# Performance work log

Measured on AMD Instinct MI355X. Metric: run time of the kernel, lower is better.

The kernel has to match this reference:

```python
import jax, jax.numpy as jnp
import numpy as np

EPS = 1e-5
N_NODES = 100000


def setup_inputs() -> dict:
    key = jax.random.key(0)
    ks = jax.random.split(key, 24)
    N, F = N_NODES, 64
    E = 1600000
    inp = {
        "x": jax.random.normal(ks[0], (N, F), dtype=jnp.float32),
        "edge_index": jax.random.randint(ks[1], (2, E), 0, N, dtype=jnp.int64),
    }
    dims = [(F, 32), (32, 64), (64, 128), (128, 1)]
    for i, (din, dout) in enumerate(dims, start=1):
        kw, kb = jax.random.split(ks[1 + i], 2)
        scale = 1.0 / np.sqrt(din)
        inp[f"W{i}"] = jax.random.uniform(kw, (din, dout), jnp.float32, -scale, scale)
        inp[f"b{i}"] = jax.random.uniform(kb, (dout,), jnp.float32, -scale, scale)
    for i, d in enumerate([32, 64, 128], start=1):
        kg, kbe, km, kv = jax.random.split(ks[8 + i], 4)
        inp[f"g{i}"] = 1.0 + 0.1 * jax.random.normal(kg, (d,), jnp.float32)
        inp[f"be{i}"] = 0.1 * jax.random.normal(kbe, (d,), jnp.float32)
        inp[f"rm{i}"] = 0.1 * jax.random.normal(km, (d,), jnp.float32)
        inp[f"rv{i}"] = 0.5 + jax.random.uniform(kv, (d,), jnp.float32)
    return inp


def _gcn_conv(x, src, dst, norm, W, b, n):
    # GCNConv: linear transform then D^-1/2 A_hat D^-1/2 aggregation (self-loops in src/dst)
    xw = x @ W  # [N, dout]
    msg = xw[src] * norm[:, None]  # [E+N, dout] gather
    return jax.ops.segment_sum(msg, dst, num_segments=n) + b


def _bn_eval(x, g, be, rm, rv):
    return (x - rm) * jax.lax.rsqrt(rv + EPS) * g + be


def reference(x, edge_index, W1, b1, W2, b2, W3, b3, W4, b4,
              g1, be1, rm1, rv1, g2, be2, rm2, rv2, g3, be3, rm3, rv3):
    n = x.shape[0]
    loop = jnp.arange(n, dtype=edge_index.dtype)
    src = jnp.concatenate([edge_index[0], loop])
    dst = jnp.concatenate([edge_index[1], loop])
    deg = jax.ops.segment_sum(jnp.ones_like(dst, dtype=x.dtype), dst, num_segments=n)
    dinv = jnp.where(deg > 0, jax.lax.rsqrt(deg), 0.0)
    norm = dinv[src] * dinv[dst]  # shared across layers

    h = _gcn_conv(x, src, dst, norm, W1, b1, n)
    h = jax.nn.elu(_bn_eval(h, g1, be1, rm1, rv1))
    h = _gcn_conv(h, src, dst, norm, W2, b2, n)
    h = jax.nn.elu(_bn_eval(h, g2, be2, rm2, rv2))
    h = _gcn_conv(h, src, dst, norm, W3, b3, n)
    h = jax.nn.elu(_bn_eval(h, g3, be3, rm3, rv3))
    h = _gcn_conv(h, src, dst, norm, W4, b4, n)
    return jax.nn.sigmoid(jax.nn.elu(h))
```

## Files before the change

kernel.cpp:

```cpp
#include <hip/hip_runtime.h>
#include <hip/hip_fp16.h>

#define EPSF 1e-5f
#define BKT_SHIFT 9
#define BKT_NODES 512
#define TILE_E 4096

typedef _Float16 half2_t __attribute__((ext_vector_type(2)));

__device__ __forceinline__ float elu_f(float x) { return x > 0.f ? x : expm1f(x); }

__device__ __forceinline__ float fdot2f(half2_t a, half2_t b, float c) {
#if __has_builtin(__builtin_amdgcn_fdot2)
    return __builtin_amdgcn_fdot2(a, b, c, false);
#else
    return c + (float)a.x * (float)b.x + (float)a.y * (float)b.y;
#endif
}
__device__ __forceinline__ half2_t bch2(unsigned u) { return __builtin_bit_cast(half2_t, u); }

__device__ __forceinline__ float4 h4_to_f4(uint2 u) {
    __half2 a = *reinterpret_cast<const __half2*>(&u.x);
    __half2 b = *reinterpret_cast<const __half2*>(&u.y);
    float2 fa = __half22float2(a);
    float2 fb = __half22float2(b);
    return make_float4(fa.x, fa.y, fb.x, fb.y);
}
__device__ __forceinline__ uint2 f4_to_h4(float4 v) {
    __half2 a = __floats2half2_rn(v.x, v.y);
    __half2 b = __floats2half2_rn(v.z, v.w);
    uint2 u;
    u.x = *reinterpret_cast<unsigned*>(&a);
    u.y = *reinterpret_cast<unsigned*>(&b);
    return u;
}


__global__ __launch_bounds__(256) void k_zero(int* p, int n) {
    int i = blockIdx.x * 256 + threadIdx.x;
    if (i < n) p[i] = 0;
}

__global__ __launch_bounds__(256) void k_bhist(const int* __restrict__ dst, int* __restrict__ bkt_cnt, int E) {
    __shared__ int h[256];
    int t = threadIdx.x;
    h[t] = 0;
    __syncthreads();
    for (long e = (long)blockIdx.x * 256 + t; e < E; e += (long)gridDim.x * 256)
        atomicAdd(&h[dst[e] >> BKT_SHIFT], 1);
    __syncthreads();
    if (h[t]) atomicAdd(&bkt_cnt[t], h[t]);
}

__global__ __launch_bounds__(256) void k_bscan(const int* __restrict__ bkt_cnt, int* __restrict__ bbase,
                                               int* __restrict__ cursor) {
    __shared__ int sh[256];
    int t = threadIdx.x;
    int v = bkt_cnt[t];
    sh[t] = v;
    __syncthreads();
    for (int off = 1; off < 256; off <<= 1) {
        int add = (t >= off) ? sh[t - off] : 0;
        __syncthreads();
        sh[t] += add;
        __syncthreads();
    }
    int ex = sh[t] - v;
    bbase[t] = ex;
    cursor[t] = ex;
}

__global__ __launch_bounds__(256) void k_bpart(const int* __restrict__ src, const int* __restrict__ dst,
                                               int* __restrict__ cursor, int2* __restrict__ csr_tmp, int E) {
    __shared__ int hcnt[256];
    __shared__ int gbase[256];
    int t = threadIdx.x;
    long tile0 = (long)blockIdx.x * TILE_E;
    hcnt[t] = 0;
    __syncthreads();
    int d[16], s[16], rk[16];
    #pragma unroll
    for (int j = 0; j < 16; ++j) {
        long e = tile0 + j * 256 + t;
        if (e < E) {
            d[j] = dst[e];
            s[j] = src[e];
            rk[j] = atomicAdd(&hcnt[d[j] >> BKT_SHIFT], 1);
        }
    }
    __syncthreads();
    int c = hcnt[t];
    if (c) gbase[t] = atomicAdd(&cursor[t], c);
    __syncthreads();
    #pragma unroll
    for (int j = 0; j < 16; ++j) {
        long e = tile0 + j * 256 + t;
        if (e < E) {
            int2 q;
            q.x = d[j];
            q.y = s[j];
            csr_tmp[gbase[d[j] >> BKT_SHIFT] + rk[j]] = q;
        }
    }
}

__global__ __launch_bounds__(256) void k_bfine(const int2* __restrict__ csr_tmp, const int* __restrict__ bbase,
                                               const int* __restrict__ bkt_cnt, int* __restrict__ cnt,
                                               int* __restrict__ base, float* __restrict__ dinv,
                                               int* __restrict__ csr_s, int N) {
    __shared__ int cnt5[BKT_NODES];
    __shared__ int off5[BKT_NODES];
    __shared__ int sh[256];
    int b = blockIdx.x;
    int t = threadIdx.x;
    int d0 = b << BKT_SHIFT;
    int bb = bbase[b];
    int bc = bkt_cnt[b];
    cnt5[t] = 0;
    cnt5[t + 256] = 0;
    __syncthreads();
    for (int k = t; k < bc; k += 256) atomicAdd(&cnt5[csr_tmp[bb + k].x - d0], 1);
    __syncthreads();
    int v0 = cnt5[2 * t], v1 = cnt5[2 * t + 1];
    int p = v0 + v1;
    sh[t] = p;
    __syncthreads();
    for (int off = 1; off < 256; off <<= 1) {
        int add = (t >= off) ? sh[t - off] : 0;
        __syncthreads();
        sh[t] += add;
        __syncthreads();
    }
    int pre = sh[t] - p;
    off5[2 * t] = pre;
    off5[2 * t + 1] = pre + v0;
    #pragma unroll
    for (int j = 0; j < 2; ++j) {
        int idx = 2 * t + j;
        int i = d0 + idx;
        if (i < N) {
            int c = cnt5[idx];
            base[i] = bb + off5[idx];
            cnt[i] = c;
            dinv[i] = rsqrtf((float)(c + 1));
        }
    }
    __syncthreads();
    for (int k = t; k < bc; k += 256) {
        int2 e = csr_tmp[bb + k];
        int pos = bb + atomicAdd(&off5[e.x - d0], 1);
        csr_s[pos] = e.y;
    }
}

template<int F, bool L1EPI, bool HIN, bool HOUT>
__global__ __launch_bounds__(256) void k_gather(const int* __restrict__ base, const int* __restrict__ cnt,
                                                const int* __restrict__ csr_s,
                                                const float* __restrict__ dinv, const void* __restrict__ xin,
                                                const float* __restrict__ b, const float* __restrict__ g,
                                                const float* __restrict__ be, const float* __restrict__ rm,
                                                const float* __restrict__ rv, void* __restrict__ out, int n) {
    constexpr int C = F / 4;
    constexpr int NPB = 256 / C;
    int lane = threadIdx.x % C;
    int nl = threadIdx.x / C;
    int i = blockIdx.x * NPB + nl;
    if (i >= n) return;
    int k = base[i];
    int kend = k + cnt[i];
    float di = dinv[i];
    const float4* XF = reinterpret_cast<const float4*>(xin);
    const uint2*  XH = reinterpret_cast<const uint2*>(xin);
    float4 z = {0.f, 0.f, 0.f, 0.f};
    float4 a0 = z, a1 = z, a2 = z, a3 = z;
    for (; k + 3 < kend; k += 4) {
        int s0 = csr_s[k], s1 = csr_s[k + 1], s2 = csr_s[k + 2], s3 = csr_s[k + 3];
        float4 x0 = HIN ? h4_to_f4(XH[(long)s0 * C + lane]) : XF[(long)s0 * C + lane];
        float4 x1 = HIN ? h4_to_f4(XH[(long)s1 * C + lane]) : XF[(long)s1 * C + lane];
        float4 x2 = HIN ? h4_to_f4(XH[(long)s2 * C + lane]) : XF[(long)s2 * C + lane];
        float4 x3 = HIN ? h4_to_f4(XH[(long)s3 * C + lane]) : XF[(long)s3 * C + lane];
        a0.x += x0.x; a0.y += x0.y; a0.z += x0.z; a0.w += x0.w;
        a1.x += x1.x; a1.y += x1.y; a1.z += x1.z; a1.w += x1.w;
        a2.x += x2.x; a2.y += x2.y; a2.z += x2.z; a2.w += x2.w;
        a3.x += x3.x; a3.y += x3.y; a3.z += x3.z; a3.w += x3.w;
    }
    for (; k < kend; ++k) {
        int s0 = csr_s[k];
        float4 xa = HIN ? h4_to_f4(XH[(long)s0 * C + lane]) : XF[(long)s0 * C + lane];
        a0.x += xa.x; a0.y += xa.y; a0.z += xa.z; a0.w += xa.w;
    }
    float4 xs = HIN ? h4_to_f4(XH[(long)i * C + lane]) : XF[(long)i * C + lane];
    float4 o;
    o.x = di * (a0.x + a1.x + a2.x + a3.x + xs.x);
    o.y = di * (a0.y + a1.y + a2.y + a3.y + xs.y);
    o.z = di * (a0.z + a1.z + a2.z + a3.z + xs.z);
    o.w = di * (a0.w + a1.w + a2.w + a3.w + xs.w);
    if (L1EPI) {
        float4 bb = reinterpret_cast<const float4*>(b)[lane];
        float4 gg = reinterpret_cast<const float4*>(g)[lane];
        float4 ee = reinterpret_cast<const float4*>(be)[lane];
        float4 mm = reinterpret_cast<const float4*>(rm)[lane];
        float4 vv = reinterpret_cast<const float4*>(rv)[lane];
        o.x = di * elu_f((o.x + bb.x - mm.x) * rsqrtf(vv.x + EPSF) * gg.x + ee.x);
        o.y = di * elu_f((o.y + bb.y - mm.y) * rsqrtf(vv.y + EPSF) * gg.y + ee.y);
        o.z = di * elu_f((o.z + bb.z - mm.z) * rsqrtf(vv.z + EPSF) * gg.z + ee.z);
        o.w = di * elu_f((o.w + bb.w - mm.w) * rsqrtf(vv.w + EPSF) * gg.w + ee.w);
    }
    if (HOUT) reinterpret_cast<uint2*>(out)[(long)i * C + lane] = f4_to_h4(o);
    else      reinterpret_cast<float4*>(out)[(long)i * C + lane] = o;
}

__global__ __launch_bounds__(256) void k_gather1_final(const int* __restrict__ base, const int* __restrict__ cnt,
                                                       const int* __restrict__ csr_s,
                                                       const float* __restrict__ dinv, const float* __restrict__ y,
                                                       const float* __restrict__ b4, float* __restrict__ out, int n) {
    int i = blockIdx.x * 256 + threadIdx.x;
    if (i >= n) return;
    int k = base[i];
    int kend = k + cnt[i];
    float di = dinv[i];
    float acc = 0.f;
    for (; k < kend; ++k) acc += y[csr_s[k]];
    float v = di * (acc + y[i]) + b4[0];
    v = elu_f(v);
    out[i] = 1.f / (1.f + expf(-v));
}

template<int DIN, int DOUT, bool BN, bool FUSE_DOT, bool SCALE_DINV, bool HOUT>
__global__ __launch_bounds__(256, 4) void k_gemm_rt(const float* __restrict__ X, const float* __restrict__ W,
                                                    const float* __restrict__ b, const float* __restrict__ g,
                                                    const float* __restrict__ be, const float* __restrict__ rm,
                                                    const float* __restrict__ rv, const float* __restrict__ W4,
                                                    const float* __restrict__ dinv,
                                                    void* __restrict__ Y, int n) {
    constexpr int TR = 4;
    constexpr int FL = DOUT / 4;
    constexpr int RG = 256 / FL;
    constexpr int BR = RG * TR;
    __shared__ float Wl[DIN * DOUT];
    for (int idx = threadIdx.x; idx < DIN * DOUT; idx += 256) Wl[idx] = W[idx];
    __syncthreads();
    const int fl = threadIdx.x % FL;
    const int rg = threadIdx.x / FL;
    const int f0 = fl * 4;
    const long r0 = (long)blockIdx.x * BR + (long)rg * TR;

    float4 z; z.x = z.y = z.z = z.w = 0.f;
    float4 acc[TR];
    #pragma unroll
    for (int r = 0; r < TR; ++r) acc[r] = z;

    #pragma unroll 2
    for (int k0 = 0; k0 < DIN; k0 += 4) {
        float4 xv[TR];
        #pragma unroll
        for (int r = 0; r < TR; ++r) {
            long row = r0 + r;
            xv[r] = (row < n) ? *reinterpret_cast<const float4*>(X + row * DIN + k0) : z;
        }
        #pragma unroll
        for (int kk = 0; kk < 4; ++kk) {
            float4 w4 = *reinterpret_cast<const float4*>(&Wl[(k0 + kk) * DOUT + f0]);
            #pragma unroll
            for (int r = 0; r < TR; ++r) {
                float xs = (kk == 0) ? xv[r].x : (kk == 1) ? xv[r].y : (kk == 2) ? xv[r].z : xv[r].w;
                acc[r].x += xs * w4.x;
                acc[r].y += xs * w4.y;
                acc[r].z += xs * w4.z;
                acc[r].w += xs * w4.w;
            }
        }
    }

    float4 bias = z, scale = z, shift = z, w4d = z;
    if (BN) {
        bias = *reinterpret_cast<const float4*>(b + f0);
        float4 gg = *reinterpret_cast<const float4*>(g + f0);
        float4 ee = *reinterpret_cast<const float4*>(be + f0);
        float4 mm = *reinterpret_cast<const float4*>(rm + f0);
        float4 vv = *reinterpret_cast<const float4*>(rv + f0);
        scale.x = gg.x * rsqrtf(vv.x + EPSF); shift.x = ee.x - mm.x * scale.x;
        scale.y = gg.y * rsqrtf(vv.y + EPSF); shift.y = ee.y - mm.y * scale.y;
        scale.z = gg.z * rsqrtf(vv.z + EPSF); shift.z = ee.z - mm.z * scale.z;
        scale.w = gg.w * rsqrtf(vv.w + EPSF); shift.w = ee.w - mm.w * scale.w;
    }
    if (FUSE_DOT) w4d = *reinterpret_cast<const float4*>(W4 + f0);

    #pragma unroll
    for (int r = 0; r < TR; ++r) {
        long row = r0 + r;
        if (row >= n) continue;
        float4 v = acc[r];
        if (BN) {
            v.x = elu_f((v.x + bias.x) * scale.x + shift.x);
            v.y = elu_f((v.y + bias.y) * scale.y + shift.y);
            v.z = elu_f((v.z + bias.z) * scale.z + shift.z);
            v.w = elu_f((v.w + bias.w) * scale.w + shift.w);
        }
        float dv = SCALE_DINV ? dinv[row] : 1.f;
        if (FUSE_DOT) {
            float p = v.x * w4d.x + v.y * w4d.y + v.z * w4d.z + v.w * w4d.w;
            #pragma unroll
            for (int m = 1; m < FL; m <<= 1) p += __shfl_xor(p, m, 64);
            if (fl == 0) reinterpret_cast<float*>(Y)[row] = dv * p;
        } else {
            if (SCALE_DINV) { v.x *= dv; v.y *= dv; v.z *= dv; v.w *= dv; }
            if (HOUT) reinterpret_cast<uint2*>(Y)[row * FL + fl] = f4_to_h4(v);
            else      *reinterpret_cast<float4*>(reinterpret_cast<float*>(Y) + row * DOUT + f0) = v;
        }
    }
}

__global__ __launch_bounds__(256, 4) void k_fuse2(const int* __restrict__ base, const int* __restrict__ cnt,
                                                  const int* __restrict__ csr_s, const float* __restrict__ dinv,
                                                  const uint2* __restrict__ Xh,
                                                  const float* __restrict__ W, const float* __restrict__ b,
                                                  const float* __restrict__ g, const float* __restrict__ be,
                                                  const float* __restrict__ rm, const float* __restrict__ rv,
                                                  uint2* __restrict__ Y,
                                                  int n) {
    __shared__ half2_t Wl2[16 * 64];
    __shared__ __align__(16) uint2 T2[32 * 8];
    __shared__ float Dl[32];
    int t = threadIdx.x;
    for (int idx = t; idx < 16 * 64; idx += 256) {
        int p = idx >> 6, j = idx & 63;
        half2_t w;
        w.x = (_Float16)W[(2 * p) * 64 + j];
        w.y = (_Float16)W[(2 * p + 1) * 64 + j];
        Wl2[idx] = w;
    }
    int lane = t & 7, nl = t >> 3;
    long i = (long)blockIdx.x * 32 + nl;
    float4 z = {0.f, 0.f, 0.f, 0.f};
    float4 o = z;
    float di = 0.f;
    if (i < n) {
        int k = base[i], kend = k + cnt[i];
        di = dinv[i];
        float4 a0 = z, a1 = z;
        for (; k + 1 < kend; k += 2) {
            int s0 = csr_s[k], s1 = csr_s[k + 1];
            float4 x0 = h4_to_f4(Xh[(long)s0 * 8 + lane]);
            float4 x1 = h4_to_f4(Xh[(long)s1 * 8 + lane]);
            a0.x += x0.x; a0.y += x0.y; a0.z += x0.z; a0.w += x0.w;
            a1.x += x1.x; a1.y += x1.y; a1.z += x1.z; a1.w += x1.w;
        }
        if (k < kend) {
            float4 xa = h4_to_f4(Xh[(long)csr_s[k] * 8 + lane]);
            a0.x += xa.x; a0.y += xa.y; a0.z += xa.z; a0.w += xa.w;
        }
        float4 xs = h4_to_f4(Xh[(long)i * 8 + lane]);
        o.x = di * (a0.x + a1.x + xs.x);
        o.y = di * (a0.y + a1.y + xs.y);
        o.z = di * (a0.z + a1.z + xs.z);
        o.w = di * (a0.w + a1.w + xs.w);
    }
    T2[nl * 8 + lane] = f4_to_h4(o);
    if (lane == 0) Dl[nl] = di;
    __syncthreads();

    int fl = t & 15, rg = t >> 4;
    int f0 = fl * 4;
    const uint4* T4 = reinterpret_cast<const uint4*>(T2);
    float4 acc0 = z, acc1 = z;
    #pragma unroll
    for (int c = 0; c < 4; ++c) {
        uint4 ra = T4[(rg * 2 + 0) * 4 + c];
        uint4 rb = T4[(rg * 2 + 1) * 4 + c];
        #pragma unroll
        for (int q = 0; q < 4; ++q) {
            uint4 wv = *reinterpret_cast<const uint4*>(&Wl2[(c * 4 + q) * 64 + f0]);
            half2_t w0 = bch2(wv.x), w1 = bch2(wv.y), w2 = bch2(wv.z), w3 = bch2(wv.w);
            unsigned ua = (q == 0) ? ra.x : (q == 1) ? ra.y : (q == 2) ? ra.z : ra.w;
            unsigned ub = (q == 0) ? rb.x : (q == 1) ? rb.y : (q == 2) ? rb.z : rb.w;
            half2_t xa = bch2(ua), xb = bch2(ub);
            acc0.x = fdot2f(xa, w0, acc0.x); acc0.y = fdot2f(xa, w1, acc0.y);
            acc0.z = fdot2f(xa, w2, acc0.z); acc0.w = fdot2f(xa, w3, acc0.w);
            acc1.x = fdot2f(xb, w0, acc1.x); acc1.y = fdot2f(xb, w1, acc1.y);
            acc1.z = fdot2f(xb, w2, acc1.z); acc1.w = fdot2f(xb, w3, acc1.w);
        }
    }
    float4 bias = *reinterpret_cast<const float4*>(b + f0);
    float4 gg = *reinterpret_cast<const float4*>(g + f0);
    float4 ee = *reinterpret_cast<const float4*>(be + f0);
    float4 mm = *reinterpret_cast<const float4*>(rm + f0);
    float4 vv = *reinterpret_cast<const float4*>(rv + f0);
    float4 scale, shift;
    scale.x = gg.x * rsqrtf(vv.x + EPSF); shift.x = ee.x - mm.x * scale.x;
    scale.y = gg.y * rsqrtf(vv.y + EPSF); shift.y = ee.y - mm.y * scale.y;
    scale.z = gg.z * rsqrtf(vv.z + EPSF); shift.z = ee.z - mm.z * scale.z;
    scale.w = gg.w * rsqrtf(vv.w + EPSF); shift.w = ee.w - mm.w * scale.w;
    #pragma unroll
    for (int r = 0; r < 2; ++r) {
        long row = (long)blockIdx.x * 32 + rg * 2 + r;
        if (row >= n) continue;
        float4 v = r ? acc1 : acc0;
        float dv = Dl[rg * 2 + r];
        v.x = dv * elu_f((v.x + bias.x) * scale.x + shift.x);
        v.y = dv * elu_f((v.y + bias.y) * scale.y + shift.y);
        v.z = dv * elu_f((v.z + bias.z) * scale.z + shift.z);
        v.w = dv * elu_f((v.w + bias.w) * scale.w + shift.w);
        Y[row * 16 + fl] = f4_to_h4(v);
    }
}

__global__ __launch_bounds__(256, 4) void k_fuse3(const int* __restrict__ base, const int* __restrict__ cnt,
                                                  const int* __restrict__ csr_s, const float* __restrict__ dinv,
                                                  const uint4* __restrict__ Xh,
                                                  const float* __restrict__ W, const float* __restrict__ b,
                                                  const float* __restrict__ g, const float* __restrict__ be,
                                                  const float* __restrict__ rm, const float* __restrict__ rv,
                                                  const float* __restrict__ W4,
                                                  float* __restrict__ y, int n) {
    __shared__ half2_t Wl2[32 * 128];
    __shared__ uint4 T3[32 * 8];
    __shared__ float Dl[32];
    int t = threadIdx.x;
    for (int idx = t; idx < 32 * 128; idx += 256) {
        int p = idx >> 7, j = idx & 127;
        half2_t w;
        w.x = (_Float16)W[(2 * p) * 128 + j];
        w.y = (_Float16)W[(2 * p + 1) * 128 + j];
        Wl2[idx] = w;
    }
    int lane = t & 7, nl = t >> 3;
    long i = (long)blockIdx.x * 32 + nl;
    float4 z = {0.f, 0.f, 0.f, 0.f};
    float4 oLo = z, oHi = z;
    float di = 0.f;
    if (i < n) {
        int k = base[i], kend = k + cnt[i];
        di = dinv[i];
        float4 aL0 = z, aH0 = z, aL1 = z, aH1 = z;
        for (; k + 1 < kend; k += 2) {
            int s0 = csr_s[k], s1 = csr_s[k + 1];
            uint4 u0 = Xh[(long)s0 * 8 + lane];
            uint4 u1 = Xh[(long)s1 * 8 + lane];
            float4 l0 = h4_to_f4(make_uint2(u0.x, u0.y)), h0 = h4_to_f4(make_uint2(u0.z, u0.w));
            float4 l1 = h4_to_f4(make_uint2(u1.x, u1.y)), h1 = h4_to_f4(make_uint2(u1.z, u1.w));
            aL0.x += l0.x; aL0.y += l0.y; aL0.z += l0.z; aL0.w += l0.w;
            aH0.x += h0.x; aH0.y += h0.y; aH0.z += h0.z; aH0.w += h0.w;
            aL1.x += l1.x; aL1.y += l1.y; aL1.z += l1.z; aL1.w += l1.w;
            aH1.x += h1.x; aH1.y += h1.y; aH1.z += h1.z; aH1.w += h1.w;
        }
        if (k < kend) {
            uint4 u0 = Xh[(long)csr_s[k] * 8 + lane];
            float4 l0 = h4_to_f4(make_uint2(u0.x, u0.y)), h0 = h4_to_f4(make_uint2(u0.z, u0.w));
            aL0.x += l0.x; aL0.y += l0.y; aL0.z += l0.z; aL0.w += l0.w;
            aH0.x += h0.x; aH0.y += h0.y; aH0.z += h0.z; aH0.w += h0.w;
        }
        uint4 us = Xh[(long)i * 8 + lane];
        float4 ls = h4_to_f4(make_uint2(us.x, us.y)), hs = h4_to_f4(make_uint2(us.z, us.w));
        oLo.x = di * (aL0.x + aL1.x + ls.x);
        oLo.y = di * (aL0.y + aL1.y + ls.y);
        oLo.z = di * (aL0.z + aL1.z + ls.z);
        oLo.w = di * (aL0.w + aL1.w + ls.w);
        oHi.x = di * (aH0.x + aH1.x + hs.x);
        oHi.y = di * (aH0.y + aH1.y + hs.y);
        oHi.z = di * (aH0.z + aH1.z + hs.z);
        oHi.w = di * (aH0.w + aH1.w + hs.w);
    }
    uint2 pl = f4_to_h4(oLo), ph = f4_to_h4(oHi);
    uint4 packed; packed.x = pl.x; packed.y = pl.y; packed.z = ph.x; packed.w = ph.y;
    T3[nl * 8 + lane] = packed;
    if (lane == 0) Dl[nl] = di;
    __syncthreads();

    int fl = t & 31, rg = t >> 5;
    int f0 = fl * 4;
    float4 acc[4] = {z, z, z, z};
    #pragma unroll 2
    for (int c = 0; c < 8; ++c) {
        uint4 rowc[4];
        #pragma unroll
        for (int r = 0; r < 4; ++r) rowc[r] = T3[(rg * 4 + r) * 8 + c];
        #pragma unroll
        for (int q = 0; q < 4; ++q) {
            uint4 wv = *reinterpret_cast<const uint4*>(&Wl2[(c * 4 + q) * 128 + f0]);
            half2_t w0 = bch2(wv.x), w1 = bch2(wv.y), w2 = bch2(wv.z), w3 = bch2(wv.w);
            #pragma unroll
            for (int r = 0; r < 4; ++r) {
                unsigned xu = (q == 0) ? rowc[r].x : (q == 1) ? rowc[r].y : (q == 2) ? rowc[r].z : rowc[r].w;
                half2_t xp = bch2(xu);
                acc[r].x = fdot2f(xp, w0, acc[r].x);
                acc[r].y = fdot2f(xp, w1, acc[r].y);
                acc[r].z = fdot2f(xp, w2, acc[r].z);
                acc[r].w = fdot2f(xp, w3, acc[r].w);
            }
        }
    }
    float4 bias = *reinterpret_cast<const float4*>(b + f0);
    float4 gg = *reinterpret_cast<const float4*>(g + f0);
    float4 ee = *reinterpret_cast<const float4*>(be + f0);
    float4 mm = *reinterpret_cast<const float4*>(rm + f0);
    float4 vv = *reinterpret_cast<const float4*>(rv + f0);
    float4 w4d = *reinterpret_cast<const float4*>(W4 + f0);
    float4 scale, shift;
    scale.x = gg.x * rsqrtf(vv.x + EPSF); shift.x = ee.x - mm.x * scale.x;
    scale.y = gg.y * rsqrtf(vv.y + EPSF); shift.y = ee.y - mm.y * scale.y;
    scale.z = gg.z * rsqrtf(vv.z + EPSF); shift.z = ee.z - mm.z * scale.z;
    scale.w = gg.w * rsqrtf(vv.w + EPSF); shift.w = ee.w - mm.w * scale.w;
    #pragma unroll
    for (int r = 0; r < 4; ++r) {
        long row = (long)blockIdx.x * 32 + rg * 4 + r;
        if (row >= n) continue;
        float4 v = acc[r];
        v.x = elu_f((v.x + bias.x) * scale.x + shift.x);
        v.y = elu_f((v.y + bias.y) * scale.y + shift.y);
        v.z = elu_f((v.z + bias.z) * scale.z + shift.z);
        v.w = elu_f((v.w + bias.w) * scale.w + shift.w);
        float p = v.x * w4d.x + v.y * w4d.y + v.z * w4d.z + v.w * w4d.w;
        #pragma unroll
        for (int m = 1; m < 32; m <<= 1) p += __shfl_xor(p, m, 64);
        if (fl == 0) y[row] = Dl[rg * 4 + r] * p;
    }
}


extern "C" void kernel_launch(void* const* d_in, const int* in_sizes, int n_in,
                              void* d_out, int out_size, void* d_ws, size_t ws_size,
                              hipStream_t stream) {
    const float* x   = (const float*)d_in[0];
    const int*   edg = (const int*)d_in[1];
    const float* W1 = (const float*)d_in[2];
    const float* b1 = (const float*)d_in[3];
    const float* W2 = (const float*)d_in[4];
    const float* b2 = (const float*)d_in[5];
    const float* W3 = (const float*)d_in[6];
    const float* b3 = (const float*)d_in[7];
    const float* W4 = (const float*)d_in[8];
    const float* b4 = (const float*)d_in[9];
    const float* g1  = (const float*)d_in[10];
    const float* be1 = (const float*)d_in[11];
    const float* rm1 = (const float*)d_in[12];
    const float* rv1 = (const float*)d_in[13];
    const float* g2  = (const float*)d_in[14];
    const float* be2 = (const float*)d_in[15];
    const float* rm2 = (const float*)d_in[16];
    const float* rv2 = (const float*)d_in[17];
    const float* g3  = (const float*)d_in[18];
    const float* be3 = (const float*)d_in[19];
    const float* rm3 = (const float*)d_in[20];
    const float* rv3 = (const float*)d_in[21];
    float* out = (float*)d_out;

    const int N = in_sizes[0] / 64;
    const int E = in_sizes[1] / 2;
    const int* src = edg;
    const int* dst = edg + E;
    const int NB_BKT = (N + BKT_NODES - 1) / BKT_NODES;
    const int NTILES = (E + TILE_E - 1) / TILE_E;

    int*   bkt_cnt = (int*)d_ws;
    int*   bbase   = bkt_cnt + 256;
    int*   cursor  = bbase + 256;
    int*   cnt     = cursor + 256;
    int*   base    = cnt + N;
    float* dinv    = (float*)(base + N);
    int*   csr_s   = (int*)(dinv + N);
    float* featA   = (float*)(csr_s + E);
    float* featB   = featA + (size_t)N * 64;
    int2*  csr_tmp = (int2*)featA;

    auto nb = [](long total) { return (int)((total + 255) / 256); };

    k_zero<<<1, 256, 0, stream>>>(bkt_cnt, 256);
    k_bhist<<<512, 256, 0, stream>>>(dst, bkt_cnt, E);
    k_bscan<<<1, 256, 0, stream>>>(bkt_cnt, bbase, cursor);
    k_bpart<<<NTILES, 256, 0, stream>>>(src, dst, cursor, csr_tmp, E);
    k_bfine<<<NB_BKT, 256, 0, stream>>>(csr_tmp, bbase, bkt_cnt, cnt, base, dinv, csr_s, N);

    k_gemm_rt<64, 32, false, false, true, true><<<(N + 127) / 128, 256, 0, stream>>>(
        x, W1, nullptr, nullptr, nullptr, nullptr, nullptr, nullptr, dinv, featB, N);
    k_gather<32, true, true, true><<<(N + 31) / 32, 256, 0, stream>>>(base, cnt, csr_s, dinv, featB,
                                                                      b1, g1, be1, rm1, rv1, featA, N);

    k_fuse2<<<(N + 31) / 32, 256, 0, stream>>>(base, cnt, csr_s, dinv, (const uint2*)featA,
                                               W2, b2, g2, be2, rm2, rv2, (uint2*)featB, N);

    k_fuse3<<<(N + 31) / 32, 256, 0, stream>>>(base, cnt, csr_s, dinv, (const uint4*)featB,
                                               W3, b3, g3, be3, rm3, rv3, W4, featA, N);

    k_gather1_final<<<nb(N), 256, 0, stream>>>(base, cnt, csr_s, dinv, featA, b4, out, N);
}
```

Baseline: 343.9 us.

## Accumulate gathers in packed fp16 and pack partition records into one word

The neighbor-sum loops in the layer-1 gather, fuse2 and fuse3 now add neighbor rows directly in packed half vectors with four accumulators, instead of converting each row to fp32 first. This removes per-element conversions and halves accumulator register use. The bucket partition temp array now stores one 32-bit word per edge (local dst in the high bits, src in the low 18 bits) instead of an int2, which halves that array's traffic. The gemm and gather templates are reduced to specialized kernels. Summing in fp16 risks precision loss and overflow on high-degree nodes, and the 18-bit src field assumes fewer than 262144 nodes.

```diff
diff --git a/kernel.cpp b/kernel.cpp
--- a/kernel.cpp
+++ b/kernel.cpp
@@ -7,6 +7,8 @@
 #define TILE_E 4096
 
 typedef _Float16 half2_t __attribute__((ext_vector_type(2)));
+typedef _Float16 half4_t __attribute__((ext_vector_type(4)));
+typedef _Float16 half8_t __attribute__((ext_vector_type(8)));
 
 __device__ __forceinline__ float elu_f(float x) { return x > 0.f ? x : expm1f(x); }
 
@@ -18,14 +20,9 @@
 #endif
 }
 __device__ __forceinline__ half2_t bch2(unsigned u) { return __builtin_bit_cast(half2_t, u); }
-
-__device__ __forceinline__ float4 h4_to_f4(uint2 u) {
-    __half2 a = *reinterpret_cast<const __half2*>(&u.x);
-    __half2 b = *reinterpret_cast<const __half2*>(&u.y);
-    float2 fa = __half22float2(a);
-    float2 fb = __half22float2(b);
-    return make_float4(fa.x, fa.y, fb.x, fb.y);
-}
+__device__ __forceinline__ half4_t bch4(uint2 u) { return __builtin_bit_cast(half4_t, u); }
+__device__ __forceinline__ half8_t bch8(uint4 u) { return __builtin_bit_cast(half8_t, u); }
+
 __device__ __forceinline__ uint2 f4_to_h4(float4 v) {
     __half2 a = __floats2half2_rn(v.x, v.y);
     __half2 b = __floats2half2_rn(v.z, v.w);
@@ -71,7 +68,7 @@
 }
 
 __global__ __launch_bounds__(256) void k_bpart(const int* __restrict__ src, const int* __restrict__ dst,
-                                               int* __restrict__ cursor, int2* __restrict__ csr_tmp, int E) {
+                                               int* __restrict__ cursor, unsigned* __restrict__ csr_tmp, int E) {
     __shared__ int hcnt[256];
     __shared__ int gbase[256];
     int t = threadIdx.x;
@@ -96,15 +93,13 @@
     for (int j = 0; j < 16; ++j) {
         long e = tile0 + j * 256 + t;
         if (e < E) {
-            int2 q;
-            q.x = d[j];
-            q.y = s[j];
-            csr_tmp[gbase[d[j] >> BKT_SHIFT] + rk[j]] = q;
-        }
-    }
-}
-
-__global__ __launch_bounds__(256) void k_bfine(const int2* __restrict__ csr_tmp, const int* __restrict__ bbase,
+            unsigned pk = ((unsigned)(d[j] & (BKT_NODES - 1)) << 18) | (unsigned)s[j];
+            csr_tmp[gbase[d[j] >> BKT_SHIFT] + rk[j]] = pk;
+        }
+    }
+}
+
+__global__ __launch_bounds__(256) void k_bfine(const unsigned* __restrict__ csr_tmp, const int* __restrict__ bbase,
                                                const int* __restrict__ bkt_cnt, int* __restrict__ cnt,
                                                int* __restrict__ base, float* __restrict__ dinv,
                                                int* __restrict__ csr_s, int N) {
@@ -119,7 +114,7 @@
     cnt5[t] = 0;
     cnt5[t + 256] = 0;
     __syncthreads();
-    for (int k = t; k < bc; k += 256) atomicAdd(&cnt5[csr_tmp[bb + k].x - d0], 1);
+    for (int k = t; k < bc; k += 256) atomicAdd(&cnt5[csr_tmp[bb + k] >> 18], 1);
     __syncthreads();
     int v0 = cnt5[2 * t], v1 = cnt5[2 * t + 1];
     int p = v0 + v1;
@@ -147,67 +142,48 @@
     }
     __syncthreads();
     for (int k = t; k < bc; k += 256) {
-        int2 e = csr_tmp[bb + k];
-        int pos = bb + atomicAdd(&off5[e.x - d0], 1);
-        csr_s[pos] = e.y;
-    }
-}
-
-template<int F, bool L1EPI, bool HIN, bool HOUT>
-__global__ __launch_bounds__(256) void k_gather(const int* __restrict__ base, const int* __restrict__ cnt,
-                                                const int* __restrict__ csr_s,
-                                                const float* __restrict__ dinv, const void* __restrict__ xin,
-                                                const float* __restrict__ b, const float* __restrict__ g,
-                                                const float* __restrict__ be, const float* __restrict__ rm,
-                                                const float* __restrict__ rv, void* __restrict__ out, int n) {
-    constexpr int C = F / 4;
-    constexpr int NPB = 256 / C;
-    int lane = threadIdx.x % C;
-    int nl = threadIdx.x / C;
-    int i = blockIdx.x * NPB + nl;
+        unsigned e = csr_tmp[bb + k];
+        int pos = bb + atomicAdd(&off5[e >> 18], 1);
+        csr_s[pos] = (int)(e & 0x3FFFFu);
+    }
+}
+
+__global__ __launch_bounds__(256) void k_gath1(const int* __restrict__ base, const int* __restrict__ cnt,
+                                               const int* __restrict__ csr_s, const float* __restrict__ dinv,
+                                               const uint2* __restrict__ Xh,
+                                               const float* __restrict__ b, const float* __restrict__ g,
+                                               const float* __restrict__ be, const float* __restrict__ rm,
+                                               const float* __restrict__ rv, uint2* __restrict__ out, int n) {
+    int lane = threadIdx.x & 7, nl = threadIdx.x >> 3;
+    long i = (long)blockIdx.x * 32 + nl;
     if (i >= n) return;
-    int k = base[i];
-    int kend = k + cnt[i];
+    int k = base[i], kend = k + cnt[i];
     float di = dinv[i];
-    const float4* XF = reinterpret_cast<const float4*>(xin);
-    const uint2*  XH = reinterpret_cast<const uint2*>(xin);
-    float4 z = {0.f, 0.f, 0.f, 0.f};
-    float4 a0 = z, a1 = z, a2 = z, a3 = z;
+    half4_t a0 = {0, 0, 0, 0}, a1 = a0, a2 = a0, a3 = a0;
     for (; k + 3 < kend; k += 4) {
         int s0 = csr_s[k], s1 = csr_s[k + 1], s2 = csr_s[k + 2], s3 = csr_s[k + 3];
-        float4 x0 = HIN ? h4_to_f4(XH[(long)s0 * C + lane]) : XF[(long)s0 * C + lane];
-        float4 x1 = HIN ? h4_to_f4(XH[(long)s1 * C + lane]) : XF[(long)s1 * C + lane];
-        float4 x2 = HIN ? h4_to_f4(XH[(long)s2 * C + lane]) : XF[(long)s2 * C + lane];
-        float4 x3 = HIN ? h4_to_f4(XH[(long)s3 * C + lane]) : XF[(long)s3 * C + lane];
-        a0.x += x0.x; a0.y += x0.y; a0.z += x0.z; a0.w += x0.w;
-        a1.x += x1.x; a1.y += x1.y; a1.z += x1.z; a1.w += x1.w;
-        a2.x += x2.x; a2.y += x2.y; a2.z += x2.z; a2.w += x2.w;
-        a3.x += x3.x; a3.y += x3.y; a3.z += x3.z; a3.w += x3.w;
-    }
-    for (; k < kend; ++k) {
-        int s0 = csr_s[k];
-        float4 xa = HIN ? h4_to_f4(XH[(long)s0 * C + lane]) : XF[(long)s0 * C + lane];
-        a0.x += xa.x; a0.y += xa.y; a0.z += xa.z; a0.w += xa.w;
-    }
-    float4 xs = HIN ? h4_to_f4(XH[(long)i * C + lane]) : XF[(long)i * C + lane];
+        a0 += bch4(Xh[(long)s0 * 8 + lane]);
+        a1 += bch4(Xh[(long)s1 * 8 + lane]);
+        a2 += bch4(Xh[(long)s2 * 8 + lane]);
+        a3 += bch4(Xh[(long)s3 * 8 + lane]);
+    }
+    for (; k < kend; ++k) a0 += bch4(Xh[(long)csr_s[k] * 8 + lane]);
+    half4_t s4 = ((a0 + a1) + (a2 + a3)) + bch4(Xh[i * 8 + lane]);
     float4 o;
-    o.x = di * (a0.x + a1.x + a2.x + a3.x + xs.x);
-    o.y = di * (a0.y + a1.y + a2.y + a3.y + xs.y);
-    o.z = di * (a0.z + a1.z + a2.z + a3.z + xs.z);
-    o.w = di * (a0.w + a1.w + a2.w + a3.w + xs.w);
-    if (L1EPI) {
-        float4 bb = reinterpret_cast<const float4*>(b)[lane];
-        float4 gg = reinterpret_cast<const float4*>(g)[lane];
-        float4 ee = reinterpret_cast<const float4*>(be)[lane];
-        float4 mm = reinterpret_cast<const float4*>(rm)[lane];
-        float4 vv = reinterpret_cast<const float4*>(rv)[lane];
-        o.x = di * elu_f((o.x + bb.x - mm.x) * rsqrtf(vv.x + EPSF) * gg.x + ee.x);
-        o.y = di * elu_f((o.y + bb.y - mm.y) * rsqrtf(vv.y + EPSF) * gg.y + ee.y);
-        o.z = di * elu_f((o.z + bb.z - mm.z) * rsqrtf(vv.z + EPSF) * gg.z + ee.z);
-        o.w = di * elu_f((o.w + bb.w - mm.w) * rsqrtf(vv.w + EPSF) * gg.w + ee.w);
-    }
-    if (HOUT) reinterpret_cast<uint2*>(out)[(long)i * C + lane] = f4_to_h4(o);
-    else      reinterpret_cast<float4*>(out)[(long)i * C + lane] = o;
+    o.x = di * (float)s4[0];
+    o.y = di * (float)s4[1];
+    o.z = di * (float)s4[2];
+    o.w = di * (float)s4[3];
+    float4 bb = reinterpret_cast<const float4*>(b)[lane];
+    float4 gg = reinterpret_cast<const float4*>(g)[lane];
+    float4 ee = reinterpret_cast<const float4*>(be)[lane];
+    float4 mm = reinterpret_cast<const float4*>(rm)[lane];
+    float4 vv = reinterpret_cast<const float4*>(rv)[lane];
+    o.x = di * elu_f((o.x + bb.x - mm.x) * rsqrtf(vv.x + EPSF) * gg.x + ee.x);
+    o.y = di * elu_f((o.y + bb.y - mm.y) * rsqrtf(vv.y + EPSF) * gg.y + ee.y);
+    o.z = di * elu_f((o.z + bb.z - mm.z) * rsqrtf(vv.z + EPSF) * gg.z + ee.z);
+    o.w = di * elu_f((o.w + bb.w - mm.w) * rsqrtf(vv.w + EPSF) * gg.w + ee.w);
+    out[i * 8 + lane] = f4_to_h4(o);
 }
 
 __global__ __launch_bounds__(256) void k_gather1_final(const int* __restrict__ base, const int* __restrict__ cnt,
@@ -226,13 +202,9 @@
     out[i] = 1.f / (1.f + expf(-v));
 }
 
-template<int DIN, int DOUT, bool BN, bool FUSE_DOT, bool SCALE_DINV, bool HOUT>
-__global__ __launch_bounds__(256, 4) void k_gemm_rt(const float* __restrict__ X, const float* __restrict__ W,
-                                                    const float* __restrict__ b, const float* __restrict__ g,
-                                                    const float* __restrict__ be, const float* __restrict__ rm,
-                                                    const float* __restrict__ rv, const float* __restrict__ W4,
-                                                    const float* __restrict__ dinv,
-                                                    void* __restrict__ Y, int n) {
+template<int DIN, int DOUT>
+__global__ __launch_bounds__(256, 4) void k_gemm1(const float* __restrict__ X, const float* __restrict__ W,
+                                                  const float* __restrict__ dinv, uint2* __restrict__ Y, int n) {
     constexpr int TR = 4;
     constexpr int FL = DOUT / 4;
     constexpr int RG = 256 / FL;
@@ -271,43 +243,14 @@
             }
         }
     }
-
-    float4 bias = z, scale = z, shift = z, w4d = z;
-    if (BN) {
-        bias = *reinterpret_cast<const float4*>(b + f0);
-        float4 gg = *reinterpret_cast<const float4*>(g + f0);
-        float4 ee = *reinterpret_cast<const float4*>(be + f0);
-        float4 mm = *reinterpret_cast<const float4*>(rm + f0);
-        float4 vv = *reinterpret_cast<const float4*>(rv + f0);
-        scale.x = gg.x * rsqrtf(vv.x + EPSF); shift.x = ee.x - mm.x * scale.x;
-        scale.y = gg.y * rsqrtf(vv.y + EPSF); shift.y = ee.y - mm.y * scale.y;
-        scale.z = gg.z * rsqrtf(vv.z + EPSF); shift.z = ee.z - mm.z * scale.z;
-        scale.w = gg.w * rsqrtf(vv.w + EPSF); shift.w = ee.w - mm.w * scale.w;
-    }
-    if (FUSE_DOT) w4d = *reinterpret_cast<const float4*>(W4 + f0);
-
     #pragma unroll
     for (int r = 0; r < TR; ++r) {
         long row = r0 + r;
         if (row >= n) continue;
+        float dv = dinv[row];
         float4 v = acc[r];
-        if (BN) {
-            v.x = elu_f((v.x + bias.x) * scale.x + shift.x);
-            v.y = elu_f((v.y + bias.y) * scale.y + shift.y);
-            v.z = elu_f((v.z + bias.z) * scale.z + shift.z);
-            v.w = elu_f((v.w + bias.w) * scale.w + shift.w);
-        }
-        float dv = SCALE_DINV ? dinv[row] : 1.f;
-        if (FUSE_DOT) {
-            float p = v.x * w4d.x + v.y * w4d.y + v.z * w4d.z + v.w * w4d.w;
-            #pragma unroll
-            for (int m = 1; m < FL; m <<= 1) p += __shfl_xor(p, m, 64);
-            if (fl == 0) reinterpret_cast<float*>(Y)[row] = dv * p;
-        } else {
-            if (SCALE_DINV) { v.x *= dv; v.y *= dv; v.z *= dv; v.w *= dv; }
-            if (HOUT) reinterpret_cast<uint2*>(Y)[row * FL + fl] = f4_to_h4(v);
-            else      *reinterpret_cast<float4*>(reinterpret_cast<float*>(Y) + row * DOUT + f0) = v;
-        }
+        v.x *= dv; v.y *= dv; v.z *= dv; v.w *= dv;
+        Y[row * FL + fl] = f4_to_h4(v);
     }
 }
 
@@ -338,23 +281,20 @@
     if (i < n) {
         int k = base[i], kend = k + cnt[i];
         di = dinv[i];
-        float4 a0 = z, a1 = z;
-        for (; k + 1 < kend; k += 2) {
-            int s0 = csr_s[k], s1 = csr_s[k + 1];
-            float4 x0 = h4_to_f4(Xh[(long)s0 * 8 + lane]);
-            float4 x1 = h4_to_f4(Xh[(long)s1 * 8 + lane]);
-            a0.x += x0.x; a0.y += x0.y; a0.z += x0.z; a0.w += x0.w;
-            a1.x += x1.x; a1.y += x1.y; a1.z += x1.z; a1.w += x1.w;
-        }
-        if (k < kend) {
-            float4 xa = h4_to_f4(Xh[(long)csr_s[k] * 8 + lane]);
-            a0.x += xa.x; a0.y += xa.y; a0.z += xa.z; a0.w += xa.w;
-        }
-        float4 xs = h4_to_f4(Xh[(long)i * 8 + lane]);
-        o.x = di * (a0.x + a1.x + xs.x);
-        o.y = di * (a0.y + a1.y + xs.y);
-        o.z = di * (a0.z + a1.z + xs.z);
-        o.w = di * (a0.w + a1.w + xs.w);
+        half4_t a0 = {0, 0, 0, 0}, a1 = a0, a2 = a0, a3 = a0;
+        for (; k + 3 < kend; k += 4) {
+            int s0 = csr_s[k], s1 = csr_s[k + 1], s2 = csr_s[k + 2], s3 = csr_s[k + 3];
+            a0 += bch4(Xh[(long)s0 * 8 + lane]);
+            a1 += bch4(Xh[(long)s1 * 8 + lane]);
+            a2 += bch4(Xh[(long)s2 * 8 + lane]);
+            a3 += bch4(Xh[(long)s3 * 8 + lane]);
+        }
+        for (; k < kend; ++k) a0 += bch4(Xh[(long)csr_s[k] * 8 + lane]);
+        half4_t s4 = ((a0 + a1) + (a2 + a3)) + bch4(Xh[i * 8 + lane]);
+        o.x = di * (float)s4[0];
+        o.y = di * (float)s4[1];
+        o.z = di * (float)s4[2];
+        o.w = di * (float)s4[3];
     }
     T2[nl * 8 + lane] = f4_to_h4(o);
     if (lane == 0) Dl[nl] = di;
@@ -432,34 +372,20 @@
     if (i < n) {
         int k = base[i], kend = k + cnt[i];
         di = dinv[i];
-        float4 aL0 = z, aH0 = z, aL1 = z, aH1 = z;
-        for (; k + 1 < kend; k += 2) {
-            int s0 = csr_s[k], s1 = csr_s[k + 1];
-            uint4 u0 = Xh[(long)s0 * 8 + lane];
-            uint4 u1 = Xh[(long)s1 * 8 + lane];
-            float4 l0 = h4_to_f4(make_uint2(u0.x, u0.y)), h0 = h4_to_f4(make_uint2(u0.z, u0.w));
-            float4 l1 = h4_to_f4(make_uint2(u1.x, u1.y)), h1 = h4_to_f4(make_uint2(u1.z, u1.w));
-            aL0.x += l0.x; aL0.y += l0.y; aL0.z += l0.z; aL0.w += l0.w;
-            aH0.x += h0.x; aH0.y += h0.y; aH0.z += h0.z; aH0.w += h0.w;
-            aL1.x += l1.x; aL1.y += l1.y; aL1.z += l1.z; aL1.w += l1.w;
-            aH1.x += h1.x; aH1.y += h1.y; aH1.z += h1.z; aH1.w += h1.w;
-        }
-        if (k < kend) {
-            uint4 u0 = Xh[(long)csr_s[k] * 8 + lane];
-            float4 l0 = h4_to_f4(make_uint2(u0.x, u0.y)), h0 = h4_to_f4(make_uint2(u0.z, u0.w));
-            aL0.x += l0.x; aL0.y += l0.y; aL0.z += l0.z; aL0.w += l0.w;
-            aH0.x += h0.x; aH0.y += h0.y; aH0.z += h0.z; aH0.w += h0.w;
-        }
-        uint4 us = Xh[(long)i * 8 + lane];
-        float4 ls = h4_to_f4(make_uint2(us.x, us.y)), hs = h4_to_f4(make_uint2(us.z, us.w));
-        oLo.x = di * (aL0.x + aL1.x + ls.x);
-        oLo.y = di * (aL0.y + aL1.y + ls.y);
-        oLo.z = di * (aL0.z + aL1.z + ls.z);
-        oLo.w = di * (aL0.w + aL1.w + ls.w);
-        oHi.x = di * (aH0.x + aH1.x + hs.x);
-        oHi.y = di * (aH0.y + aH1.y + hs.y);
-        oHi.z = di * (aH0.z + aH1.z + hs.z);
-        oHi.w = di * (aH0.w + aH1.w + hs.w);
+        half8_t a0 = {0, 0, 0, 0, 0, 0, 0, 0}, a1 = a0, a2 = a0, a3 = a0;
+        for (; k + 3 < kend; k += 4) {
+            int s0 = csr_s[k], s1 = csr_s[k + 1], s2 = csr_s[k + 2], s3 = csr_s[k + 3];
+            a0 += bch8(Xh[(long)s0 * 8 + lane]);
+            a1 += bch8(Xh[(long)s1 * 8 + lane]);
+            a2 += bch8(Xh[(long)s2 * 8 + lane]);
+            a3 += bch8(Xh[(long)s3 * 8 + lane]);
+        }
+        for (; k < kend; ++k) a0 += bch8(Xh[(long)csr_s[k] * 8 + lane]);
+        half8_t s8 = ((a0 + a1) + (a2 + a3)) + bch8(Xh[i * 8 + lane]);
+        oLo.x = di * (float)s8[0]; oLo.y = di * (float)s8[1];
+        oLo.z = di * (float)s8[2]; oLo.w = di * (float)s8[3];
+        oHi.x = di * (float)s8[4]; oHi.y = di * (float)s8[5];
+        oHi.z = di * (float)s8[6]; oHi.w = di * (float)s8[7];
     }
     uint2 pl = f4_to_h4(oLo), ph = f4_to_h4(oHi);
     uint4 packed; packed.x = pl.x; packed.y = pl.y; packed.z = ph.x; packed.w = ph.y;
@@ -552,16 +478,16 @@
     const int NB_BKT = (N + BKT_NODES - 1) / BKT_NODES;
     const int NTILES = (E + TILE_E - 1) / TILE_E;
 
-    int*   bkt_cnt = (int*)d_ws;
-    int*   bbase   = bkt_cnt + 256;
-    int*   cursor  = bbase + 256;
-    int*   cnt     = cursor + 256;
-    int*   base    = cnt + N;
-    float* dinv    = (float*)(base + N);
-    int*   csr_s   = (int*)(dinv + N);
-    float* featA   = (float*)(csr_s + E);
-    float* featB   = featA + (size_t)N * 64;
-    int2*  csr_tmp = (int2*)featA;
+    int*      bkt_cnt = (int*)d_ws;
+    int*      bbase   = bkt_cnt + 256;
+    int*      cursor  = bbase + 256;
+    int*      cnt     = cursor + 256;
+    int*      base    = cnt + N;
+    float*    dinv    = (float*)(base + N);
+    int*      csr_s   = (int*)(dinv + N);
+    float*    featA   = (float*)(csr_s + E);
+    float*    featB   = featA + (size_t)N * 64;
+    unsigned* csr_tmp = (unsigned*)featA;
 
     auto nb = [](long total) { return (int)((total + 255) / 256); };
 
@@ -571,10 +497,9 @@
     k_bpart<<<NTILES, 256, 0, stream>>>(src, dst, cursor, csr_tmp, E);
     k_bfine<<<NB_BKT, 256, 0, stream>>>(csr_tmp, bbase, bkt_cnt, cnt, base, dinv, csr_s, N);
 
-    k_gemm_rt<64, 32, false, false, true, true><<<(N + 127) / 128, 256, 0, stream>>>(
-        x, W1, nullptr, nullptr, nullptr, nullptr, nullptr, nullptr, dinv, featB, N);
-    k_gather<32, true, true, true><<<(N + 31) / 32, 256, 0, stream>>>(base, cnt, csr_s, dinv, featB,
-                                                                      b1, g1, be1, rm1, rv1, featA, N);
+    k_gemm1<64, 32><<<(N + 127) / 128, 256, 0, stream>>>(x, W1, dinv, (uint2*)featB, N);
+    k_gath1<<<(N + 31) / 32, 256, 0, stream>>>(base, cnt, csr_s, dinv, (const uint2*)featB,
+                                               b1, g1, be1, rm1, rv1, (uint2*)featA, N);
 
     k_fuse2<<<(N + 31) / 32, 256, 0, stream>>>(base, cnt, csr_s, dinv, (const uint2*)featA,
                                                W2, b2, g2, be2, rm2, rv2, (uint2*)featB, N);
```

Result: no change. 339.3 us (-1.3%).
